# Performance work log

Measured on AMD Instinct MI355X. Metric: run time of the kernel, lower is better.

Reference implementation:

```python
import jax, jax.numpy as jnp
import numpy as np

B = 8192
N = 722          # number of independent tiny MLPs
CAM = 10         # CAMERA_VECTOR_DIM
IN = CAM + 1     # per-MLP input dim
H = 10           # hidden dim
LOD = 6          # NUM_LOD_LEVELS


def setup_inputs() -> dict:
    key = jax.random.key(0)
    ks = jax.random.split(key, 8)
    return {
        "prior_lod": jax.random.uniform(ks[0], (B, N), dtype=jnp.float32),
        "camera": jax.random.normal(ks[1], (B, CAM), dtype=jnp.float32),
        "W1": jax.random.normal(ks[2], (N, IN, H), dtype=jnp.float32) * 0.3,
        "b1": jax.random.normal(ks[3], (N, H), dtype=jnp.float32) * 0.1,
        "W2": jax.random.normal(ks[4], (N, H, H), dtype=jnp.float32) * 0.3,
        "b2": jax.random.normal(ks[5], (N, H), dtype=jnp.float32) * 0.1,
        "W3": jax.random.normal(ks[6], (N, H, LOD), dtype=jnp.float32) * 0.3,
        "b3": jax.random.normal(ks[7], (N, LOD), dtype=jnp.float32) * 0.1,
    }


def reference(prior_lod, camera, W1, b1, W2, b2, W3, b3):
    # Per-network input: cat(prior_lod[:, i:i+1], camera) -> [B, N, IN]
    cam = jnp.broadcast_to(camera[:, None, :], (prior_lod.shape[0], W1.shape[0], camera.shape[1]))
    x = jnp.concatenate([prior_lod[:, :, None], cam], axis=-1)  # [B, N, IN]
    # Batched 3-layer MLP over the N axis (grouped GEMM equivalent of the 722-loop)
    h = jax.nn.relu(jnp.einsum('bni,nih->bnh', x, W1) + b1[None])   # [B, N, H]
    h = jax.nn.relu(jnp.einsum('bnh,nhk->bnk', h, W2) + b2[None])   # [B, N, H]
    out = jnp.einsum('bnh,nho->bno', h, W3) + b3[None]              # [B, N, LOD]
    return out  # stacked version of the original list of 722 [B, LOD] outputs
```

## Files before the change

kernel.cpp:

```cpp
#include <hip/hip_runtime.h>


#define NN 722
#define CAMD 10
#define HD 10
#define LODD 6
#define ROWF (NN * LODD)
#define SUB 4
#define BT 256
#define NETS_PER_CHUNK 4
#define NCHUNKS 181
#define CPG 2
#define NGROUPS 91
#define LSTRIDE 25
#define HROWS 128

__device__ __forceinline__ void lds_barrier() {
    asm volatile("s_waitcnt lgkmcnt(0)" ::: "memory");
    __builtin_amdgcn_s_barrier();
}

__global__ __launch_bounds__(256) void Net_18966575579675_kernel(
    const float* __restrict__ prior, const float* __restrict__ camera,
    const float* __restrict__ W1, const float* __restrict__ b1,
    const float* __restrict__ W2, const float* __restrict__ b2,
    const float* __restrict__ W3, const float* __restrict__ b3,
    float* __restrict__ out)
{
    const int tid  = threadIdx.x;
    const int lane = tid & 63;
    const int wave = __builtin_amdgcn_readfirstlane(tid >> 6);
    const int b0   = blockIdx.x * BT;

    const int c_begin = blockIdx.y * CPG;
    const int c_end   = (c_begin + CPG < NCHUNKS) ? (c_begin + CPG) : NCHUNKS;

    __shared__ float cam_lds[CAMD][BT];
    __shared__ float obuf[HROWS * LSTRIDE];

    {
        const float2* c2 = (const float2*)(camera + (size_t)(b0 + tid) * CAMD);
#pragma unroll
        for (int i = 0; i < CAMD / 2; ++i) {
            float2 v = c2[i];
            cam_lds[2 * i][tid]     = v.x;
            cam_lds[2 * i + 1][tid] = v.y;
        }
    }

    float pr0, pr1, pr2, pr3;
    {
        const int n0 = c_begin * NETS_PER_CHUNK + wave;
        const int nc = n0 < NN ? n0 : NN - 1;
        pr0 = prior[(size_t)(b0 + 0 * 64 + lane) * NN + nc];
        pr1 = prior[(size_t)(b0 + 1 * 64 + lane) * NN + nc];
        pr2 = prior[(size_t)(b0 + 2 * 64 + lane) * NN + nc];
        pr3 = prior[(size_t)(b0 + 3 * 64 + lane) * NN + nc];
    }

    lds_barrier();

    for (int c = c_begin; c < c_end; ++c) {
        const int n   = c * NETS_PER_CHUNK + wave;
        const bool act = (n < NN);
        const int nc  = act ? n : NN - 1;

        const float* __restrict__ w1 = W1 + (size_t)nc * (CAMD + 1) * HD;
        const float* __restrict__ p1 = b1 + (size_t)nc * HD;
        const float* __restrict__ w2 = W2 + (size_t)nc * HD * HD;
        const float* __restrict__ p2 = b2 + (size_t)nc * HD;
        const float* __restrict__ w3 = W3 + (size_t)nc * HD * LODD;
        const float* __restrict__ p3 = b3 + (size_t)nc * LODD;

        float prn0 = pr0, prn1 = pr1, prn2 = pr2, prn3 = pr3;
        if (c + 1 < c_end) {
            const int n1 = (c + 1) * NETS_PER_CHUNK + wave;
            const int nx = n1 < NN ? n1 : NN - 1;
            prn0 = prior[(size_t)(b0 + 0 * 64 + lane) * NN + nx];
            prn1 = prior[(size_t)(b0 + 1 * 64 + lane) * NN + nx];
            prn2 = prior[(size_t)(b0 + 2 * 64 + lane) * NN + nx];
            prn3 = prior[(size_t)(b0 + 3 * 64 + lane) * NN + nx];
        }

        const int rem = NN - c * NETS_PER_CHUNK;
        const int nv  = rem < NETS_PER_CHUNK ? rem : NETS_PER_CHUNK;

#pragma unroll 1
        for (int s = 0; s < SUB; ++s) {
            if (act) {
                const int row = s * 64 + lane;
                const float prs = (s == 0) ? pr0 : (s == 1) ? pr1
                                  : (s == 2) ? pr2 : pr3;

                float cv[CAMD];
#pragma unroll
                for (int i = 0; i < CAMD; ++i)
                    cv[i] = cam_lds[i][row];

                float h1[HD];
#pragma unroll
                for (int j = 0; j < HD; ++j)
                    h1[j] = fmaf(prs, w1[j], p1[j]);
#pragma unroll
                for (int i = 0; i < CAMD; ++i)
#pragma unroll
                    for (int j = 0; j < HD; ++j)
                        h1[j] = fmaf(cv[i], w1[(i + 1) * HD + j], h1[j]);
#pragma unroll
                for (int j = 0; j < HD; ++j)
                    h1[j] = fmaxf(h1[j], 0.0f);

                float h2[HD];
#pragma unroll
                for (int k = 0; k < HD; ++k)
                    h2[k] = p2[k];
#pragma unroll
                for (int j = 0; j < HD; ++j)
#pragma unroll
                    for (int k = 0; k < HD; ++k)
                        h2[k] = fmaf(h1[j], w2[j * HD + k], h2[k]);
#pragma unroll
                for (int k = 0; k < HD; ++k)
                    h2[k] = fmaxf(h2[k], 0.0f);

                float o[LODD];
#pragma unroll
                for (int m = 0; m < LODD; ++m)
                    o[m] = p3[m];
#pragma unroll
                for (int j = 0; j < HD; ++j)
#pragma unroll
                    for (int m = 0; m < LODD; ++m)
                        o[m] = fmaf(h2[j], w3[j * LODD + m], o[m]);

                const int lrow = (s & 1) * 64 + lane;
#pragma unroll
                for (int m = 0; m < LODD; ++m)
                    obuf[lrow * LSTRIDE + wave * LODD + m] = o[m];
            }

            if (s & 1) {
                lds_barrier();
                const int h = s >> 1;
                if (nv == NETS_PER_CHUNK) {
                    for (int f = tid; f < HROWS * 6; f += 256) {
                        const int row  = f / 6;
                        const int colq = f - row * 6;
                        const float* sp = obuf + row * LSTRIDE + colq * 4;
                        float4 v = make_float4(sp[0], sp[1], sp[2], sp[3]);
                        *(float4*)(out + (size_t)(b0 + h * HROWS + row) * ROWF
                                   + c * (NETS_PER_CHUNK * LODD) + colq * 4) = v;
                    }
                } else {
                    for (int f = tid; f < HROWS * 3; f += 256) {
                        const int row  = f / 3;
                        const int colq = f - row * 3;
                        const float* sp = obuf + row * LSTRIDE + colq * 4;
                        float4 v = make_float4(sp[0], sp[1], sp[2], sp[3]);
                        *(float4*)(out + (size_t)(b0 + h * HROWS + row) * ROWF
                                   + c * (NETS_PER_CHUNK * LODD) + colq * 4) = v;
                    }
                }
                lds_barrier();
            }
        }

        pr0 = prn0; pr1 = prn1; pr2 = prn2; pr3 = prn3;
    }
}

extern "C" void kernel_launch(void* const* d_in, const int* in_sizes, int n_in,
                              void* d_out, int out_size, void* d_ws, size_t ws_size,
                              hipStream_t stream) {
    const float* prior  = (const float*)d_in[0];
    const float* camera = (const float*)d_in[1];
    const float* W1     = (const float*)d_in[2];
    const float* b1     = (const float*)d_in[3];
    const float* W2     = (const float*)d_in[4];
    const float* b2     = (const float*)d_in[5];
    const float* W3     = (const float*)d_in[6];
    const float* b3     = (const float*)d_in[7];
    float* out = (float*)d_out;

    dim3 grid(8192 / BT, NGROUPS);
    dim3 block(256);
    Net_18966575579675_kernel<<<grid, block, 0, stream>>>(
        prior, camera, W1, b1, W2, b2, W3, b3, out);
}
```

Measured before the change: 250.4 us.

## Process two nets and two row halves per wave with register tiling

Each wave now computes two networks on two 64-row slices at once, with rows per block cut to 128 and eight nets per pair. Each weight load is then reused across four FMAs, which amortises the scalar weight loads and exposes more independent FMA chains. Output rows become 48 floats wide, giving longer contiguous stores and fewer barrier rounds per output byte. The cost is higher register pressure that may reduce occupancy, and the grid shape changes to 64x46.

```diff
diff --git a/kernel.cpp b/kernel.cpp
--- a/kernel.cpp
+++ b/kernel.cpp
@@ -6,14 +6,11 @@
 #define HD 10
 #define LODD 6
 #define ROWF (NN * LODD)
-#define SUB 4
-#define BT 256
-#define NETS_PER_CHUNK 4
-#define NCHUNKS 181
-#define CPG 2
-#define NGROUPS 91
-#define LSTRIDE 25
-#define HROWS 128
+#define ROWS 128
+#define NPAIRS 91
+#define PPB 2
+#define GY 46
+#define LSTRIDE 49
 
 __device__ __forceinline__ void lds_barrier() {
     asm volatile("s_waitcnt lgkmcnt(0)" ::: "memory");
@@ -30,15 +27,15 @@
     const int tid  = threadIdx.x;
     const int lane = tid & 63;
     const int wave = __builtin_amdgcn_readfirstlane(tid >> 6);
-    const int b0   = blockIdx.x * BT;
-
-    const int c_begin = blockIdx.y * CPG;
-    const int c_end   = (c_begin + CPG < NCHUNKS) ? (c_begin + CPG) : NCHUNKS;
-
-    __shared__ float cam_lds[CAMD][BT];
-    __shared__ float obuf[HROWS * LSTRIDE];
-
-    {
+    const int b0   = blockIdx.x * ROWS;
+
+    const int p_begin = blockIdx.y * PPB;
+    const int p_end   = (p_begin + PPB < NPAIRS) ? (p_begin + PPB) : NPAIRS;
+
+    __shared__ float cam_lds[CAMD][ROWS];
+    __shared__ float obuf[ROWS * LSTRIDE];
+
+    if (tid < ROWS) {
         const float2* c2 = (const float2*)(camera + (size_t)(b0 + tid) * CAMD);
 #pragma unroll
         for (int i = 0; i < CAMD / 2; ++i) {
@@ -48,124 +45,174 @@
         }
     }
 
-    float pr0, pr1, pr2, pr3;
+    float prA0, prA1, prB0, prB1;
     {
-        const int n0 = c_begin * NETS_PER_CHUNK + wave;
-        const int nc = n0 < NN ? n0 : NN - 1;
-        pr0 = prior[(size_t)(b0 + 0 * 64 + lane) * NN + nc];
-        pr1 = prior[(size_t)(b0 + 1 * 64 + lane) * NN + nc];
-        pr2 = prior[(size_t)(b0 + 2 * 64 + lane) * NN + nc];
-        pr3 = prior[(size_t)(b0 + 3 * 64 + lane) * NN + nc];
+        const int na = p_begin * 8 + wave;
+        const int nb = p_begin * 8 + 4 + wave;
+        const int ca = na < NN ? na : NN - 1;
+        const int cb = nb < NN ? nb : NN - 1;
+        prA0 = prior[(size_t)(b0 + lane) * NN + ca];
+        prA1 = prior[(size_t)(b0 + 64 + lane) * NN + ca];
+        prB0 = prior[(size_t)(b0 + lane) * NN + cb];
+        prB1 = prior[(size_t)(b0 + 64 + lane) * NN + cb];
     }
 
     lds_barrier();
 
-    for (int c = c_begin; c < c_end; ++c) {
-        const int n   = c * NETS_PER_CHUNK + wave;
-        const bool act = (n < NN);
-        const int nc  = act ? n : NN - 1;
-
-        const float* __restrict__ w1 = W1 + (size_t)nc * (CAMD + 1) * HD;
-        const float* __restrict__ p1 = b1 + (size_t)nc * HD;
-        const float* __restrict__ w2 = W2 + (size_t)nc * HD * HD;
-        const float* __restrict__ p2 = b2 + (size_t)nc * HD;
-        const float* __restrict__ w3 = W3 + (size_t)nc * HD * LODD;
-        const float* __restrict__ p3 = b3 + (size_t)nc * LODD;
-
-        float prn0 = pr0, prn1 = pr1, prn2 = pr2, prn3 = pr3;
-        if (c + 1 < c_end) {
-            const int n1 = (c + 1) * NETS_PER_CHUNK + wave;
-            const int nx = n1 < NN ? n1 : NN - 1;
-            prn0 = prior[(size_t)(b0 + 0 * 64 + lane) * NN + nx];
-            prn1 = prior[(size_t)(b0 + 1 * 64 + lane) * NN + nx];
-            prn2 = prior[(size_t)(b0 + 2 * 64 + lane) * NN + nx];
-            prn3 = prior[(size_t)(b0 + 3 * 64 + lane) * NN + nx];
-        }
-
-        const int rem = NN - c * NETS_PER_CHUNK;
-        const int nv  = rem < NETS_PER_CHUNK ? rem : NETS_PER_CHUNK;
-
 #pragma unroll 1
-        for (int s = 0; s < SUB; ++s) {
-            if (act) {
-                const int row = s * 64 + lane;
-                const float prs = (s == 0) ? pr0 : (s == 1) ? pr1
-                                  : (s == 2) ? pr2 : pr3;
-
-                float cv[CAMD];
-#pragma unroll
-                for (int i = 0; i < CAMD; ++i)
-                    cv[i] = cam_lds[i][row];
-
-                float h1[HD];
-#pragma unroll
-                for (int j = 0; j < HD; ++j)
-                    h1[j] = fmaf(prs, w1[j], p1[j]);
-#pragma unroll
-                for (int i = 0; i < CAMD; ++i)
-#pragma unroll
-                    for (int j = 0; j < HD; ++j)
-                        h1[j] = fmaf(cv[i], w1[(i + 1) * HD + j], h1[j]);
-#pragma unroll
-                for (int j = 0; j < HD; ++j)
-                    h1[j] = fmaxf(h1[j], 0.0f);
-
-                float h2[HD];
-#pragma unroll
-                for (int k = 0; k < HD; ++k)
-                    h2[k] = p2[k];
-#pragma unroll
-                for (int j = 0; j < HD; ++j)
-#pragma unroll
-                    for (int k = 0; k < HD; ++k)
-                        h2[k] = fmaf(h1[j], w2[j * HD + k], h2[k]);
-#pragma unroll
-                for (int k = 0; k < HD; ++k)
-                    h2[k] = fmaxf(h2[k], 0.0f);
-
-                float o[LODD];
+    for (int p = p_begin; p < p_end; ++p) {
+        if (8 * p >= NN) break;
+
+        const int naRaw = 8 * p + wave;
+        const int nbRaw = 8 * p + 4 + wave;
+        const bool actA = naRaw < NN;
+        const bool actB = nbRaw < NN;
+        const int nA = actA ? naRaw : NN - 1;
+        const int nB = actB ? nbRaw : NN - 1;
+
+        const float* __restrict__ w1A = W1 + (size_t)nA * (CAMD + 1) * HD;
+        const float* __restrict__ w1B = W1 + (size_t)nB * (CAMD + 1) * HD;
+        const float* __restrict__ p1A = b1 + (size_t)nA * HD;
+        const float* __restrict__ p1B = b1 + (size_t)nB * HD;
+        const float* __restrict__ w2A = W2 + (size_t)nA * HD * HD;
+        const float* __restrict__ w2B = W2 + (size_t)nB * HD * HD;
+        const float* __restrict__ p2A = b2 + (size_t)nA * HD;
+        const float* __restrict__ p2B = b2 + (size_t)nB * HD;
+        const float* __restrict__ w3A = W3 + (size_t)nA * HD * LODD;
+        const float* __restrict__ w3B = W3 + (size_t)nB * HD * LODD;
+        const float* __restrict__ p3A = b3 + (size_t)nA * LODD;
+        const float* __restrict__ p3B = b3 + (size_t)nB * LODD;
+
+        float nxA0 = prA0, nxA1 = prA1, nxB0 = prB0, nxB1 = prB1;
+        if (p + 1 < p_end && 8 * (p + 1) < NN) {
+            const int na2 = 8 * (p + 1) + wave;
+            const int nb2 = 8 * (p + 1) + 4 + wave;
+            const int ca2 = na2 < NN ? na2 : NN - 1;
+            const int cb2 = nb2 < NN ? nb2 : NN - 1;
+            nxA0 = prior[(size_t)(b0 + lane) * NN + ca2];
+            nxA1 = prior[(size_t)(b0 + 64 + lane) * NN + ca2];
+            nxB0 = prior[(size_t)(b0 + lane) * NN + cb2];
+            nxB1 = prior[(size_t)(b0 + 64 + lane) * NN + cb2];
+        }
+
+        float h1A[2][HD], h1B[2][HD];
+#pragma unroll
+        for (int j = 0; j < HD; ++j) {
+            const float wA = w1A[j], bA = p1A[j];
+            const float wB = w1B[j], bB = p1B[j];
+            h1A[0][j] = fmaf(prA0, wA, bA);
+            h1A[1][j] = fmaf(prA1, wA, bA);
+            h1B[0][j] = fmaf(prB0, wB, bB);
+            h1B[1][j] = fmaf(prB1, wB, bB);
+        }
+#pragma unroll
+        for (int i = 0; i < CAMD; ++i) {
+            const float c0 = cam_lds[i][lane];
+            const float c1 = cam_lds[i][64 + lane];
+#pragma unroll
+            for (int j = 0; j < HD; ++j) {
+                const float wA = w1A[(i + 1) * HD + j];
+                const float wB = w1B[(i + 1) * HD + j];
+                h1A[0][j] = fmaf(c0, wA, h1A[0][j]);
+                h1A[1][j] = fmaf(c1, wA, h1A[1][j]);
+                h1B[0][j] = fmaf(c0, wB, h1B[0][j]);
+                h1B[1][j] = fmaf(c1, wB, h1B[1][j]);
+            }
+        }
+#pragma unroll
+        for (int j = 0; j < HD; ++j) {
+            h1A[0][j] = fmaxf(h1A[0][j], 0.0f);
+            h1A[1][j] = fmaxf(h1A[1][j], 0.0f);
+            h1B[0][j] = fmaxf(h1B[0][j], 0.0f);
+            h1B[1][j] = fmaxf(h1B[1][j], 0.0f);
+        }
+
+        float h2A[2][HD], h2B[2][HD];
+#pragma unroll
+        for (int k = 0; k < HD; ++k) {
+            const float bA = p2A[k], bB = p2B[k];
+            h2A[0][k] = bA; h2A[1][k] = bA;
+            h2B[0][k] = bB; h2B[1][k] = bB;
+        }
+#pragma unroll
+        for (int j = 0; j < HD; ++j) {
+#pragma unroll
+            for (int k = 0; k < HD; ++k) {
+                const float wA = w2A[j * HD + k];
+                const float wB = w2B[j * HD + k];
+                h2A[0][k] = fmaf(h1A[0][j], wA, h2A[0][k]);
+                h2A[1][k] = fmaf(h1A[1][j], wA, h2A[1][k]);
+                h2B[0][k] = fmaf(h1B[0][j], wB, h2B[0][k]);
+                h2B[1][k] = fmaf(h1B[1][j], wB, h2B[1][k]);
+            }
+        }
+#pragma unroll
+        for (int k = 0; k < HD; ++k) {
+            h2A[0][k] = fmaxf(h2A[0][k], 0.0f);
+            h2A[1][k] = fmaxf(h2A[1][k], 0.0f);
+            h2B[0][k] = fmaxf(h2B[0][k], 0.0f);
+            h2B[1][k] = fmaxf(h2B[1][k], 0.0f);
+        }
+
+        float oA[2][LODD], oB[2][LODD];
+#pragma unroll
+        for (int m = 0; m < LODD; ++m) {
+            const float bA = p3A[m], bB = p3B[m];
+            oA[0][m] = bA; oA[1][m] = bA;
+            oB[0][m] = bB; oB[1][m] = bB;
+        }
+#pragma unroll
+        for (int j = 0; j < HD; ++j) {
+#pragma unroll
+            for (int m = 0; m < LODD; ++m) {
+                const float wA = w3A[j * LODD + m];
+                const float wB = w3B[j * LODD + m];
+                oA[0][m] = fmaf(h2A[0][j], wA, oA[0][m]);
+                oA[1][m] = fmaf(h2A[1][j], wA, oA[1][m]);
+                oB[0][m] = fmaf(h2B[0][j], wB, oB[0][m]);
+                oB[1][m] = fmaf(h2B[1][j], wB, oB[1][m]);
+            }
+        }
+
+        lds_barrier();
+
+        if (actA) {
+#pragma unroll
+            for (int s = 0; s < 2; ++s)
 #pragma unroll
                 for (int m = 0; m < LODD; ++m)
-                    o[m] = p3[m];
-#pragma unroll
-                for (int j = 0; j < HD; ++j)
-#pragma unroll
-                    for (int m = 0; m < LODD; ++m)
-                        o[m] = fmaf(h2[j], w3[j * LODD + m], o[m]);
-
-                const int lrow = (s & 1) * 64 + lane;
+                    obuf[(s * 64 + lane) * LSTRIDE + wave * LODD + m] = oA[s][m];
+        }
+        if (actB) {
+#pragma unroll
+            for (int s = 0; s < 2; ++s)
 #pragma unroll
                 for (int m = 0; m < LODD; ++m)
-                    obuf[lrow * LSTRIDE + wave * LODD + m] = o[m];
-            }
-
-            if (s & 1) {
-                lds_barrier();
-                const int h = s >> 1;
-                if (nv == NETS_PER_CHUNK) {
-                    for (int f = tid; f < HROWS * 6; f += 256) {
-                        const int row  = f / 6;
-                        const int colq = f - row * 6;
-                        const float* sp = obuf + row * LSTRIDE + colq * 4;
-                        float4 v = make_float4(sp[0], sp[1], sp[2], sp[3]);
-                        *(float4*)(out + (size_t)(b0 + h * HROWS + row) * ROWF
-                                   + c * (NETS_PER_CHUNK * LODD) + colq * 4) = v;
-                    }
-                } else {
-                    for (int f = tid; f < HROWS * 3; f += 256) {
-                        const int row  = f / 3;
-                        const int colq = f - row * 3;
-                        const float* sp = obuf + row * LSTRIDE + colq * 4;
-                        float4 v = make_float4(sp[0], sp[1], sp[2], sp[3]);
-                        *(float4*)(out + (size_t)(b0 + h * HROWS + row) * ROWF
-                                   + c * (NETS_PER_CHUNK * LODD) + colq * 4) = v;
-                    }
-                }
-                lds_barrier();
-            }
-        }
-
-        pr0 = prn0; pr1 = prn1; pr2 = prn2; pr3 = prn3;
+                    obuf[(s * 64 + lane) * LSTRIDE + 24 + wave * LODD + m] = oB[s][m];
+        }
+
+        lds_barrier();
+
+        const int rem = NN - 8 * p;
+        if (rem >= 8) {
+            for (int f = tid; f < ROWS * 12; f += 256) {
+                const int row  = f / 12;
+                const int colq = f - row * 12;
+                const float* sp = obuf + row * LSTRIDE + colq * 4;
+                float4 v = make_float4(sp[0], sp[1], sp[2], sp[3]);
+                *(float4*)(out + (size_t)(b0 + row) * ROWF + p * 48 + colq * 4) = v;
+            }
+        } else {
+            for (int f = tid; f < ROWS * 3; f += 256) {
+                const int row  = f / 3;
+                const int colq = f - row * 3;
+                const float* sp = obuf + row * LSTRIDE + colq * 4;
+                float4 v = make_float4(sp[0], sp[1], sp[2], sp[3]);
+                *(float4*)(out + (size_t)(b0 + row) * ROWF + p * 48 + colq * 4) = v;
+            }
+        }
+
+        prA0 = nxA0; prA1 = nxA1; prB0 = nxB0; prB1 = nxB1;
     }
 }
 
@@ -182,7 +229,7 @@
     const float* b3     = (const float*)d_in[7];
     float* out = (float*)d_out;
 
-    dim3 grid(8192 / BT, NGROUPS);
+    dim3 grid(8192 / ROWS, GY);
     dim3 block(256);
     Net_18966575579675_kernel<<<grid, block, 0, stream>>>(
         prior, camera, W1, b1, W2, b2, W3, b3, out);
```

New measurement: 260.7 us. 4.1% more time.

## Stage per-net weights in LDS and compute four row groups per weight load

Applied to the files above, without the earlier changes.

Each wave now copies its net's weights and biases into a double-buffered LDS region with padded, vector-aligned rows, staging the next chunk while computing the current one. The compute loop handles all four 64-row subgroups at once, so each weight vector read from LDS is reused across four rows instead of being re-read from global memory per row. Camera values are stored as float2, and launch bounds ask for four blocks per CU. The cost is much higher register pressure from the 4x10 accumulators, which may cause spills or lower occupancy. There is also no barrier between the per-wave staging writes and the reads, which works only because each wave reads only its own slice.

```diff
diff --git a/kernel.cpp b/kernel.cpp
--- a/kernel.cpp
+++ b/kernel.cpp
@@ -6,7 +6,6 @@
 #define HD 10
 #define LODD 6
 #define ROWF (NN * LODD)
-#define SUB 4
 #define BT 256
 #define NETS_PER_CHUNK 4
 #define NCHUNKS 181
@@ -15,12 +14,33 @@
 #define LSTRIDE 25
 #define HROWS 128
 
+#define NETSTRIDE 368
+#define OFF_W2 132
+#define OFF_W3 252
+#define OFF_B1 332
+#define OFF_B2 344
+#define OFF_B3 356
+
 __device__ __forceinline__ void lds_barrier() {
     asm volatile("s_waitcnt lgkmcnt(0)" ::: "memory");
     __builtin_amdgcn_s_barrier();
 }
 
-__global__ __launch_bounds__(256) void Net_18966575579675_kernel(
+#define LOAD10(dst, base) do {                                   \
+    const float4 _a = *(const float4*)(base);                    \
+    const float4 _b = *(const float4*)((base) + 4);              \
+    const float2 _c = *(const float2*)((base) + 8);              \
+    dst[0]=_a.x; dst[1]=_a.y; dst[2]=_a.z; dst[3]=_a.w;          \
+    dst[4]=_b.x; dst[5]=_b.y; dst[6]=_b.z; dst[7]=_b.w;          \
+    dst[8]=_c.x; dst[9]=_c.y; } while (0)
+
+#define LOAD6(dst, base) do {                                    \
+    const float4 _a = *(const float4*)(base);                    \
+    const float2 _c = *(const float2*)((base) + 4);              \
+    dst[0]=_a.x; dst[1]=_a.y; dst[2]=_a.z; dst[3]=_a.w;          \
+    dst[4]=_c.x; dst[5]=_c.y; } while (0)
+
+__global__ __launch_bounds__(256, 4) void Net_18966575579675_kernel(
     const float* __restrict__ prior, const float* __restrict__ camera,
     const float* __restrict__ W1, const float* __restrict__ b1,
     const float* __restrict__ W2, const float* __restrict__ b2,
@@ -35,18 +55,42 @@
     const int c_begin = blockIdx.y * CPG;
     const int c_end   = (c_begin + CPG < NCHUNKS) ? (c_begin + CPG) : NCHUNKS;
 
-    __shared__ float cam_lds[CAMD][BT];
-    __shared__ float obuf[HROWS * LSTRIDE];
+    __shared__ float2 cam2[CAMD / 2][BT];
+    __shared__ float  obuf[HROWS * LSTRIDE];
+    __shared__ __align__(16) float wbuf[2][NETS_PER_CHUNK * NETSTRIDE];
 
     {
         const float2* c2 = (const float2*)(camera + (size_t)(b0 + tid) * CAMD);
 #pragma unroll
-        for (int i = 0; i < CAMD / 2; ++i) {
-            float2 v = c2[i];
-            cam_lds[2 * i][tid]     = v.x;
-            cam_lds[2 * i + 1][tid] = v.y;
-        }
+        for (int i = 0; i < CAMD / 2; ++i)
+            cam2[i][tid] = c2[i];
     }
+
+    auto stage_now = [&](int cc) {
+        const int ns = cc * NETS_PER_CHUNK + wave;
+        if (ns < NN) {
+            float* wd = &wbuf[cc & 1][wave * NETSTRIDE];
+            const float* s1 = W1 + (size_t)ns * (CAMD + 1) * HD;
+#pragma unroll
+            for (int t0 = 0; t0 < 110; t0 += 64) {
+                const int t = t0 + lane;
+                if (t < 110) { const int i = t / 10, j = t - 10 * i; wd[i * 12 + j] = s1[t]; }
+            }
+            const float* s2 = W2 + (size_t)ns * HD * HD;
+#pragma unroll
+            for (int t0 = 0; t0 < 100; t0 += 64) {
+                const int t = t0 + lane;
+                if (t < 100) { const int j = t / 10, k = t - 10 * j; wd[OFF_W2 + j * 12 + k] = s2[t]; }
+            }
+            const float* s3 = W3 + (size_t)ns * HD * LODD;
+            if (lane < 60) { const int j = lane / 6, m = lane - 6 * j; wd[OFF_W3 + j * 8 + m] = s3[lane]; }
+            if (lane < 10)      wd[OFF_B1 + lane]      = b1[(size_t)ns * HD + lane];
+            else if (lane < 20) wd[OFF_B2 + lane - 10] = b2[(size_t)ns * HD + lane - 10];
+            else if (lane < 26) wd[OFF_B3 + lane - 20] = b3[(size_t)ns * LODD + lane - 20];
+        }
+    };
+
+    stage_now(c_begin);
 
     float pr0, pr1, pr2, pr3;
     {
@@ -60,112 +104,156 @@
 
     lds_barrier();
 
+#pragma unroll 1
     for (int c = c_begin; c < c_end; ++c) {
         const int n   = c * NETS_PER_CHUNK + wave;
         const bool act = (n < NN);
-        const int nc  = act ? n : NN - 1;
-
-        const float* __restrict__ w1 = W1 + (size_t)nc * (CAMD + 1) * HD;
-        const float* __restrict__ p1 = b1 + (size_t)nc * HD;
-        const float* __restrict__ w2 = W2 + (size_t)nc * HD * HD;
-        const float* __restrict__ p2 = b2 + (size_t)nc * HD;
-        const float* __restrict__ w3 = W3 + (size_t)nc * HD * LODD;
-        const float* __restrict__ p3 = b3 + (size_t)nc * LODD;
-
-        float prn0 = pr0, prn1 = pr1, prn2 = pr2, prn3 = pr3;
+
+        if (c + 1 < c_end) stage_now(c + 1);
+
+        float nx0 = pr0, nx1 = pr1, nx2 = pr2, nx3 = pr3;
         if (c + 1 < c_end) {
             const int n1 = (c + 1) * NETS_PER_CHUNK + wave;
-            const int nx = n1 < NN ? n1 : NN - 1;
-            prn0 = prior[(size_t)(b0 + 0 * 64 + lane) * NN + nx];
-            prn1 = prior[(size_t)(b0 + 1 * 64 + lane) * NN + nx];
-            prn2 = prior[(size_t)(b0 + 2 * 64 + lane) * NN + nx];
-            prn3 = prior[(size_t)(b0 + 3 * 64 + lane) * NN + nx];
+            const int nc = n1 < NN ? n1 : NN - 1;
+            nx0 = prior[(size_t)(b0 + 0 * 64 + lane) * NN + nc];
+            nx1 = prior[(size_t)(b0 + 1 * 64 + lane) * NN + nc];
+            nx2 = prior[(size_t)(b0 + 2 * 64 + lane) * NN + nc];
+            nx3 = prior[(size_t)(b0 + 3 * 64 + lane) * NN + nc];
+        }
+
+        float o[4][LODD];
+        if (act) {
+            const float* wb = &wbuf[c & 1][wave * NETSTRIDE];
+
+            float h1[4][HD];
+            {
+                float bv[10]; LOAD10(bv, wb + OFF_B1);
+                float wv[10]; LOAD10(wv, wb);
+#pragma unroll
+                for (int j = 0; j < HD; ++j) {
+                    h1[0][j] = fmaf(pr0, wv[j], bv[j]);
+                    h1[1][j] = fmaf(pr1, wv[j], bv[j]);
+                    h1[2][j] = fmaf(pr2, wv[j], bv[j]);
+                    h1[3][j] = fmaf(pr3, wv[j], bv[j]);
+                }
+            }
+#pragma unroll
+            for (int i2 = 0; i2 < CAMD / 2; ++i2) {
+                const float2 c0 = cam2[i2][0 * 64 + lane];
+                const float2 c1 = cam2[i2][1 * 64 + lane];
+                const float2 c2v = cam2[i2][2 * 64 + lane];
+                const float2 c3 = cam2[i2][3 * 64 + lane];
+                float wa[10]; LOAD10(wa, wb + (2 * i2 + 1) * 12);
+                float wc[10]; LOAD10(wc, wb + (2 * i2 + 2) * 12);
+#pragma unroll
+                for (int j = 0; j < HD; ++j) {
+                    h1[0][j] = fmaf(c0.x, wa[j], h1[0][j]);
+                    h1[1][j] = fmaf(c1.x, wa[j], h1[1][j]);
+                    h1[2][j] = fmaf(c2v.x, wa[j], h1[2][j]);
+                    h1[3][j] = fmaf(c3.x, wa[j], h1[3][j]);
+                }
+#pragma unroll
+                for (int j = 0; j < HD; ++j) {
+                    h1[0][j] = fmaf(c0.y, wc[j], h1[0][j]);
+                    h1[1][j] = fmaf(c1.y, wc[j], h1[1][j]);
+                    h1[2][j] = fmaf(c2v.y, wc[j], h1[2][j]);
+                    h1[3][j] = fmaf(c3.y, wc[j], h1[3][j]);
+                }
+            }
+#pragma unroll
+            for (int s = 0; s < 4; ++s)
+#pragma unroll
+                for (int j = 0; j < HD; ++j)
+                    h1[s][j] = fmaxf(h1[s][j], 0.0f);
+
+            float h2[4][HD];
+            {
+                float bv[10]; LOAD10(bv, wb + OFF_B2);
+#pragma unroll
+                for (int k = 0; k < HD; ++k) {
+                    h2[0][k] = bv[k]; h2[1][k] = bv[k];
+                    h2[2][k] = bv[k]; h2[3][k] = bv[k];
+                }
+            }
+#pragma unroll
+            for (int j = 0; j < HD; ++j) {
+                float wv[10]; LOAD10(wv, wb + OFF_W2 + j * 12);
+#pragma unroll
+                for (int k = 0; k < HD; ++k) {
+                    h2[0][k] = fmaf(h1[0][j], wv[k], h2[0][k]);
+                    h2[1][k] = fmaf(h1[1][j], wv[k], h2[1][k]);
+                    h2[2][k] = fmaf(h1[2][j], wv[k], h2[2][k]);
+                    h2[3][k] = fmaf(h1[3][j], wv[k], h2[3][k]);
+                }
+            }
+#pragma unroll
+            for (int s = 0; s < 4; ++s)
+#pragma unroll
+                for (int k = 0; k < HD; ++k)
+                    h2[s][k] = fmaxf(h2[s][k], 0.0f);
+
+            {
+                float bv[6]; LOAD6(bv, wb + OFF_B3);
+#pragma unroll
+                for (int m = 0; m < LODD; ++m) {
+                    o[0][m] = bv[m]; o[1][m] = bv[m];
+                    o[2][m] = bv[m]; o[3][m] = bv[m];
+                }
+            }
+#pragma unroll
+            for (int j = 0; j < HD; ++j) {
+                float wv[6]; LOAD6(wv, wb + OFF_W3 + j * 8);
+#pragma unroll
+                for (int m = 0; m < LODD; ++m) {
+                    o[0][m] = fmaf(h2[0][j], wv[m], o[0][m]);
+                    o[1][m] = fmaf(h2[1][j], wv[m], o[1][m]);
+                    o[2][m] = fmaf(h2[2][j], wv[m], o[2][m]);
+                    o[3][m] = fmaf(h2[3][j], wv[m], o[3][m]);
+                }
+            }
         }
 
         const int rem = NN - c * NETS_PER_CHUNK;
         const int nv  = rem < NETS_PER_CHUNK ? rem : NETS_PER_CHUNK;
 
-#pragma unroll 1
-        for (int s = 0; s < SUB; ++s) {
+#pragma unroll
+        for (int h = 0; h < 2; ++h) {
             if (act) {
-                const int row = s * 64 + lane;
-                const float prs = (s == 0) ? pr0 : (s == 1) ? pr1
-                                  : (s == 2) ? pr2 : pr3;
-
-                float cv[CAMD];
-#pragma unroll
-                for (int i = 0; i < CAMD; ++i)
-                    cv[i] = cam_lds[i][row];
-
-                float h1[HD];
-#pragma unroll
-                for (int j = 0; j < HD; ++j)
-                    h1[j] = fmaf(prs, w1[j], p1[j]);
-#pragma unroll
-                for (int i = 0; i < CAMD; ++i)
-#pragma unroll
-                    for (int j = 0; j < HD; ++j)
-                        h1[j] = fmaf(cv[i], w1[(i + 1) * HD + j], h1[j]);
-#pragma unroll
-                for (int j = 0; j < HD; ++j)
-                    h1[j] = fmaxf(h1[j], 0.0f);
-
-                float h2[HD];
-#pragma unroll
-                for (int k = 0; k < HD; ++k)
-                    h2[k] = p2[k];
-#pragma unroll
-                for (int j = 0; j < HD; ++j)
-#pragma unroll
-                    for (int k = 0; k < HD; ++k)
-                        h2[k] = fmaf(h1[j], w2[j * HD + k], h2[k]);
-#pragma unroll
-                for (int k = 0; k < HD; ++k)
-                    h2[k] = fmaxf(h2[k], 0.0f);
-
-                float o[LODD];
-#pragma unroll
-                for (int m = 0; m < LODD; ++m)
-                    o[m] = p3[m];
-#pragma unroll
-                for (int j = 0; j < HD; ++j)
+#pragma unroll
+                for (int ss = 0; ss < 2; ++ss) {
+                    const int s = 2 * h + ss;
 #pragma unroll
                     for (int m = 0; m < LODD; ++m)
-                        o[m] = fmaf(h2[j], w3[j * LODD + m], o[m]);
-
-                const int lrow = (s & 1) * 64 + lane;
-#pragma unroll
-                for (int m = 0; m < LODD; ++m)
-                    obuf[lrow * LSTRIDE + wave * LODD + m] = o[m];
-            }
-
-            if (s & 1) {
-                lds_barrier();
-                const int h = s >> 1;
-                if (nv == NETS_PER_CHUNK) {
-                    for (int f = tid; f < HROWS * 6; f += 256) {
-                        const int row  = f / 6;
-                        const int colq = f - row * 6;
-                        const float* sp = obuf + row * LSTRIDE + colq * 4;
-                        float4 v = make_float4(sp[0], sp[1], sp[2], sp[3]);
-                        *(float4*)(out + (size_t)(b0 + h * HROWS + row) * ROWF
-                                   + c * (NETS_PER_CHUNK * LODD) + colq * 4) = v;
-                    }
-                } else {
-                    for (int f = tid; f < HROWS * 3; f += 256) {
-                        const int row  = f / 3;
-                        const int colq = f - row * 3;
-                        const float* sp = obuf + row * LSTRIDE + colq * 4;
-                        float4 v = make_float4(sp[0], sp[1], sp[2], sp[3]);
-                        *(float4*)(out + (size_t)(b0 + h * HROWS + row) * ROWF
-                                   + c * (NETS_PER_CHUNK * LODD) + colq * 4) = v;
-                    }
-                }
-                lds_barrier();
-            }
-        }
-
-        pr0 = prn0; pr1 = prn1; pr2 = prn2; pr3 = prn3;
+                        obuf[(ss * 64 + lane) * LSTRIDE + wave * LODD + m] =
+                            (s == 0) ? o[0][m] : (s == 1) ? o[1][m]
+                          : (s == 2) ? o[2][m] : o[3][m];
+                }
+            }
+            lds_barrier();
+
+            if (nv == NETS_PER_CHUNK) {
+                for (int f = tid; f < HROWS * 6; f += 256) {
+                    const int row  = f / 6;
+                    const int colq = f - row * 6;
+                    const float* sp = obuf + row * LSTRIDE + colq * 4;
+                    float4 v = make_float4(sp[0], sp[1], sp[2], sp[3]);
+                    *(float4*)(out + (size_t)(b0 + h * HROWS + row) * ROWF
+                               + c * (NETS_PER_CHUNK * LODD) + colq * 4) = v;
+                }
+            } else {
+                for (int f = tid; f < HROWS * 3; f += 256) {
+                    const int row  = f / 3;
+                    const int colq = f - row * 3;
+                    const float* sp = obuf + row * LSTRIDE + colq * 4;
+                    float4 v = make_float4(sp[0], sp[1], sp[2], sp[3]);
+                    *(float4*)(out + (size_t)(b0 + h * HROWS + row) * ROWF
+                               + c * (NETS_PER_CHUNK * LODD) + colq * 4) = v;
+                }
+            }
+            lds_barrier();
+        }
+
+        pr0 = nx0; pr1 = nx1; pr2 = nx2; pr3 = nx3;
     }
 }
 
```

Result: faster. 242.0 us (-3.3%).
